# Kernel tuning notes

Measured on AMD Instinct MI355X. Metric: run time of the kernel, lower is better.

## Reference

```python
import jax, jax.numpy as jnp
import numpy as np

N = 50000
E = 400000
IN_DIM = 384
HID = 256
Q_DIM = 384
HEAD_HID = 128


def _glorot(key, shape):
    fan_in, fan_out = shape[0], shape[1]
    lim = float(np.sqrt(6.0 / (fan_in + fan_out)))
    return jax.random.uniform(key, shape, jnp.float32, -lim, lim)


def setup_inputs() -> dict:
    key = jax.random.key(0)
    ks = jax.random.split(key, 10)
    x = jax.random.normal(ks[0], (N, IN_DIM), jnp.float32)
    edge_index = jax.random.randint(ks[1], (2, E), 0, N, dtype=jnp.int64)
    q = jax.random.normal(ks[2], (Q_DIM,), jnp.float32)
    # layer 1: Linear(in_dim*2 + query_dim -> hidden)
    W1 = _glorot(ks[3], (IN_DIM * 2 + Q_DIM, HID))
    b1 = jnp.zeros((HID,), jnp.float32)
    # layer 2: Linear(hidden*2 + query_dim -> hidden)
    W2 = _glorot(ks[4], (HID * 2 + Q_DIM, HID))
    b2 = jnp.zeros((HID,), jnp.float32)
    # score head: Linear(hidden + query_dim -> 128) -> ReLU -> Linear(128 -> 1)
    Wh1 = _glorot(ks[5], (HID + Q_DIM, HEAD_HID))
    bh1 = jnp.zeros((HEAD_HID,), jnp.float32)
    Wh2 = _glorot(ks[6], (HEAD_HID, 1))
    bh2 = jnp.zeros((1,), jnp.float32)
    return {"x": x, "edge_index": edge_index, "q": q,
            "W1": W1, "b1": b1, "W2": W2, "b2": b2,
            "Wh1": Wh1, "bh1": bh1, "Wh2": Wh2, "bh2": bh2}


def _sage_layer(h, src, dst, q, W, b, n_nodes):
    # mean aggregation with self-loops: (sum_{j in N(i)} h_j + h_i) / (deg_i + 1)
    deg = jnp.zeros((n_nodes,), h.dtype).at[dst].add(1.0) + 1.0  # [N]
    agg = (jax.ops.segment_sum(h[src], dst, num_segments=n_nodes) + h) / deg[:, None]
    q_exp = jnp.broadcast_to(q, (n_nodes, q.shape[0]))
    cat = jnp.concatenate([h, agg, q_exp], axis=-1)  # [N, 2*d + q_dim]
    return jax.nn.relu(cat @ W + b)  # dropout is identity in eval mode


def reference(x, edge_index, q, W1, b1, W2, b2, Wh1, bh1, Wh2, bh2):
    src, dst = edge_index[0], edge_index[1]
    n = x.shape[0]
    h = _sage_layer(x, src, dst, q, W1, b1, n)
    h = _sage_layer(h, src, dst, q, W2, b2, n)
    q_exp = jnp.broadcast_to(q, (n, q.shape[0]))
    s = jax.nn.relu(jnp.concatenate([h, q_exp], axis=-1) @ Wh1 + bh1)
    logits = (s @ Wh2 + bh2).squeeze(-1)  # [N]
    return logits
```

## Files before the change

kernel.cpp:

```cpp
#include <hip/hip_runtime.h>
#include <cstdint>
#include <cstddef>

typedef unsigned short u16;
typedef short short8 __attribute__((ext_vector_type(8)));
typedef unsigned short u16x8 __attribute__((ext_vector_type(8)));
typedef unsigned short u16x4 __attribute__((ext_vector_type(4)));
typedef float f32x4 __attribute__((ext_vector_type(4)));

#define DEVI __device__ __forceinline__

#if defined(__has_builtin)
#if __has_builtin(__builtin_amdgcn_global_load_lds)
#define USE_GLD 1
#endif
#endif

DEVI float bf2f(u16 u) { return __uint_as_float(((unsigned)u) << 16); }
DEVI u16 f2bf(float f) {
  unsigned u = __float_as_uint(f);
  u += 0x7FFFu + ((u >> 16) & 1u);
  return (u16)(u >> 16);
}

DEVI void stage16(const u16* __restrict__ g, u16* lds_base, int lane) {
#ifdef USE_GLD
  __builtin_amdgcn_global_load_lds(
      (const __attribute__((address_space(1))) unsigned int*)g,
      (__attribute__((address_space(3))) unsigned int*)lds_base, 16, 0, 0);
#else
  *(u16x8*)(lds_base + lane * 8) = *(const u16x8*)g;
#endif
}

__global__ void build_deg(const int* __restrict__ dst, int* __restrict__ deg, int E) {
  int e = blockIdx.x * 256 + threadIdx.x;
  if (e < E) atomicAdd(&deg[dst[e]], 1);
}

__global__ __launch_bounds__(256) void scan1(const int* __restrict__ deg,
                                             int* __restrict__ pref,
                                             int* __restrict__ bsum, int Nn) {
  __shared__ int wsum[4];
  int i = blockIdx.x * 256 + threadIdx.x;
  int lane = threadIdx.x & 63, w = threadIdx.x >> 6;
  int v = (i < Nn) ? deg[i] : 0;
  int s = v;
  for (int off = 1; off < 64; off <<= 1) {
    int t = __shfl_up(s, off, 64);
    if (lane >= off) s += t;
  }
  if (lane == 63) wsum[w] = s;
  __syncthreads();
  int add = 0;
  for (int k = 0; k < w; ++k) add += wsum[k];
  int incl = s + add;
  if (i < Nn) pref[i] = incl - v;
  if (threadIdx.x == 255) bsum[blockIdx.x] = incl;
}

__global__ __launch_bounds__(256) void scan2(int* __restrict__ bsum,
                                             int* __restrict__ row_ofs,
                                             int nb, int Nn) {
  __shared__ int wsum[4];
  int t = threadIdx.x;
  int lane = t & 63, w = t >> 6;
  int v = (t < nb) ? bsum[t] : 0;
  int s = v;
  for (int off = 1; off < 64; off <<= 1) {
    int u = __shfl_up(s, off, 64);
    if (lane >= off) s += u;
  }
  if (lane == 63) wsum[w] = s;
  __syncthreads();
  int add = 0;
  for (int k = 0; k < w; ++k) add += wsum[k];
  int incl = s + add;
  if (t < nb) bsum[t] = incl - v;
  if (t == 255) row_ofs[Nn] = incl;
}

__global__ __launch_bounds__(256) void scan3(const int* __restrict__ pref,
                                             const int* __restrict__ bsum,
                                             int* __restrict__ row_ofs,
                                             int* __restrict__ cursor, int Nn) {
  int i = blockIdx.x * 256 + threadIdx.x;
  if (i < Nn) {
    int r = pref[i] + bsum[blockIdx.x];
    row_ofs[i] = r;
    cursor[i] = r;
  }
}

__global__ void csr_fill(const int* __restrict__ src, const int* __restrict__ dst,
                         int* __restrict__ cursor, int* __restrict__ col, int E) {
  int e = blockIdx.x * 256 + threadIdx.x;
  if (e < E) {
    int p = atomicAdd(&cursor[dst[e]], 1);
    col[p] = src[e];
  }
}

__global__ void pack_bt(const float* __restrict__ W, u16* __restrict__ Bt,
                        int K, int ldW, int r1) {
  int c = blockIdx.y;
  int k = blockIdx.x * 256 + threadIdx.x;
  if (k >= K) return;
  float v = (c < ldW) ? W[(size_t)k * ldW + c]
                      : W[(size_t)(r1 + k) * ldW + (c - ldW)];
  Bt[(size_t)c * K + k] = f2bf(v);
}

__global__ __launch_bounds__(384) void bias_q(
    const float* __restrict__ W, const float* __restrict__ b,
    const float* __restrict__ q, float* __restrict__ outb,
    int ld, int roff, int Kq) {
  __shared__ float part[6];
  int c = blockIdx.x;
  int t = threadIdx.x;
  float p = (t < Kq) ? q[t] * W[(size_t)(roff + t) * ld + c] : 0.0f;
  for (int off = 32; off > 0; off >>= 1) p += __shfl_down(p, off, 64);
  if ((t & 63) == 0) part[t >> 6] = p;
  __syncthreads();
  if (t == 0) {
    float acc = b[c];
    int nw = (blockDim.x + 63) >> 6;
    for (int w = 0; w < nw; ++w) acc += part[w];
    outb[c] = acc;
  }
}

#define BM 128
#define BN 128
#define BK 32


__global__ __launch_bounds__(256) void gemm_f32a(
    const float* __restrict__ A, const u16* __restrict__ Bt,
    u16* __restrict__ C, const float* __restrict__ bias,
    int M, int K, int Nc, int bias_len, int relu) {
  __shared__ __align__(16) u16 lds_a[BM * BK];
  __shared__ __align__(16) u16 lds_b[BN * BK];

  const int tid = threadIdx.x;
  const int lane = tid & 63;
  const int wave = tid >> 6;
  const int wm = wave & 1, wn = wave >> 1;
  const int row0 = blockIdx.y * BM;
  const int col0 = blockIdx.x * BN;
  const int m = lane & 15;
  const int quad = lane >> 4;
  const int csel = quad ^ ((m >> 1) & 3);

  const int rA0 = tid >> 2;
  const int rA1 = 64 + rA0;
  const int cs = tid & 3;
  const int s0 = rA0 * 4 + (cs ^ ((rA0 >> 1) & 3));
  const int s1 = rA1 * 4 + (cs ^ ((rA1 >> 1) & 3));
  int ga0 = row0 + rA0; if (ga0 >= M) ga0 = M - 1;
  int ga1 = row0 + rA1; if (ga1 >= M) ga1 = M - 1;
  const float* pa0 = A + (size_t)ga0 * K + cs * 8;
  const float* pa1 = A + (size_t)ga1 * K + cs * 8;

  const int rB0 = tid >> 2, rB1 = 64 + rB0;
  const int cB0 = (tid & 3) ^ ((rB0 >> 1) & 3);
  const int cB1 = (tid & 3) ^ ((rB1 >> 1) & 3);
  const u16* pb0 = Bt + (size_t)(col0 + rB0) * K + cB0 * 8;
  const u16* pb1 = Bt + (size_t)(col0 + rB1) * K + cB1 * 8;
  u16* ldsb_base0 = lds_b + (size_t)(wave * 64) * 8;
  u16* ldsb_base1 = lds_b + (size_t)(256 + wave * 64) * 8;

  f32x4 acc[4][4] = {};

  for (int k0 = 0; k0 < K; k0 += BK) {
    f32x4 a0a = *(const f32x4*)pa0, a0b = *(const f32x4*)(pa0 + 4); pa0 += BK;
    f32x4 a1a = *(const f32x4*)pa1, a1b = *(const f32x4*)(pa1 + 4); pa1 += BK;
    u16x8 h0, h1;
#pragma unroll
    for (int j = 0; j < 4; ++j) {
      h0[j] = f2bf(a0a[j]); h0[j + 4] = f2bf(a0b[j]);
      h1[j] = f2bf(a1a[j]); h1[j + 4] = f2bf(a1b[j]);
    }
    __syncthreads();
    stage16(pb0, ldsb_base0, lane); pb0 += BK;
    stage16(pb1, ldsb_base1, lane); pb1 += BK;
    *(u16x8*)&lds_a[s0 * 8] = h0;
    *(u16x8*)&lds_a[s1 * 8] = h1;
    __syncthreads();

    short8 af[4], bfv[4];
#pragma unroll
    for (int mt = 0; mt < 4; ++mt)
      af[mt] = *(const short8*)&lds_a[((wm * 64 + mt * 16 + m) * 4 + csel) * 8];
#pragma unroll
    for (int nt = 0; nt < 4; ++nt)
      bfv[nt] = *(const short8*)&lds_b[((wn * 64 + nt * 16 + m) * 4 + csel) * 8];
#pragma unroll
    for (int mt = 0; mt < 4; ++mt)
#pragma unroll
      for (int nt = 0; nt < 4; ++nt)
        acc[mt][nt] = __builtin_amdgcn_mfma_f32_16x16x32_bf16(
            af[mt], bfv[nt], acc[mt][nt], 0, 0, 0);
  }

#pragma unroll
  for (int nt = 0; nt < 4; ++nt) {
    int col = col0 + wn * 64 + nt * 16 + m;
    float bb = (col < bias_len) ? bias[col] : 0.0f;
#pragma unroll
    for (int mt = 0; mt < 4; ++mt)
#pragma unroll
      for (int r = 0; r < 4; ++r) {
        int row = row0 + wm * 64 + mt * 16 + quad * 4 + r;
        if (row < M) {
          float v = acc[mt][nt][r] + bb;
          if (relu) v = fmaxf(v, 0.0f);
          C[(size_t)row * Nc + col] = f2bf(v);
        }
      }
  }
}

__global__ __launch_bounds__(256) void gemm_bf16a(
    const u16* __restrict__ A, const u16* __restrict__ Bt,
    u16* __restrict__ C, const float* __restrict__ bias,
    int M, int K, int Nc, int bias_len, int relu) {
  __shared__ __align__(16) u16 lds_a[BM * BK];
  __shared__ __align__(16) u16 lds_b[BN * BK];

  const int tid = threadIdx.x;
  const int lane = tid & 63;
  const int wave = tid >> 6;
  const int wm = wave & 1, wn = wave >> 1;
  const int row0 = blockIdx.y * BM;
  const int col0 = blockIdx.x * BN;
  const int m = lane & 15;
  const int quad = lane >> 4;
  const int csel = quad ^ ((m >> 1) & 3);

  const int r0 = tid >> 2, r1 = 64 + r0;
  const int c0 = (tid & 3) ^ ((r0 >> 1) & 3);
  const int c1 = (tid & 3) ^ ((r1 >> 1) & 3);
  int ga0 = row0 + r0; if (ga0 >= M) ga0 = M - 1;
  int ga1 = row0 + r1; if (ga1 >= M) ga1 = M - 1;
  const u16* pa0 = A + (size_t)ga0 * K + c0 * 8;
  const u16* pa1 = A + (size_t)ga1 * K + c1 * 8;
  const u16* pb0 = Bt + (size_t)(col0 + r0) * K + c0 * 8;
  const u16* pb1 = Bt + (size_t)(col0 + r1) * K + c1 * 8;
  u16* la0 = lds_a + (size_t)(wave * 64) * 8;
  u16* la1 = lds_a + (size_t)(256 + wave * 64) * 8;
  u16* lb0 = lds_b + (size_t)(wave * 64) * 8;
  u16* lb1 = lds_b + (size_t)(256 + wave * 64) * 8;

  f32x4 acc[4][4] = {};

  for (int k0 = 0; k0 < K; k0 += BK) {
    __syncthreads();
    stage16(pa0, la0, lane); pa0 += BK;
    stage16(pa1, la1, lane); pa1 += BK;
    stage16(pb0, lb0, lane); pb0 += BK;
    stage16(pb1, lb1, lane); pb1 += BK;
    __syncthreads();

    short8 af[4], bfv[4];
#pragma unroll
    for (int mt = 0; mt < 4; ++mt)
      af[mt] = *(const short8*)&lds_a[((wm * 64 + mt * 16 + m) * 4 + csel) * 8];
#pragma unroll
    for (int nt = 0; nt < 4; ++nt)
      bfv[nt] = *(const short8*)&lds_b[((wn * 64 + nt * 16 + m) * 4 + csel) * 8];
#pragma unroll
    for (int mt = 0; mt < 4; ++mt)
#pragma unroll
      for (int nt = 0; nt < 4; ++nt)
        acc[mt][nt] = __builtin_amdgcn_mfma_f32_16x16x32_bf16(
            af[mt], bfv[nt], acc[mt][nt], 0, 0, 0);
  }

#pragma unroll
  for (int nt = 0; nt < 4; ++nt) {
    int col = col0 + wn * 64 + nt * 16 + m;
    float bb = (col < bias_len) ? bias[col] : 0.0f;
#pragma unroll
    for (int mt = 0; mt < 4; ++mt)
#pragma unroll
      for (int r = 0; r < 4; ++r) {
        int row = row0 + wm * 64 + mt * 16 + quad * 4 + r;
        if (row < M) {
          float v = acc[mt][nt][r] + bb;
          if (relu) v = fmaxf(v, 0.0f);
          C[(size_t)row * Nc + col] = f2bf(v);
        }
      }
  }
}

__global__ __launch_bounds__(256) void aggregate(
    const u16* __restrict__ C, const int* __restrict__ row_ofs,
    const int* __restrict__ col_idx, u16* __restrict__ H, int Nn) {
  int node = blockIdx.x * 4 + (threadIdx.x >> 6);
  if (node >= Nn) return;
  int lane = threadIdx.x & 63;
  int s = row_ofs[node], e = row_ofs[node + 1];
  float inv = 1.0f / (float)(e - s + 1);
  const u16* crow = C + (size_t)node * 512;
  u16x4 y0 = *(const u16x4*)(crow + 256 + lane * 4);
  float a0 = bf2f(y0[0]), a1 = bf2f(y0[1]), a2 = bf2f(y0[2]), a3 = bf2f(y0[3]);
  int t = s;
  for (; t + 4 <= e; t += 4) {
    int j0 = col_idx[t], j1 = col_idx[t + 1], j2 = col_idx[t + 2], j3 = col_idx[t + 3];
    u16x4 v0 = *(const u16x4*)(C + (size_t)j0 * 512 + 256 + lane * 4);
    u16x4 v1 = *(const u16x4*)(C + (size_t)j1 * 512 + 256 + lane * 4);
    u16x4 v2 = *(const u16x4*)(C + (size_t)j2 * 512 + 256 + lane * 4);
    u16x4 v3 = *(const u16x4*)(C + (size_t)j3 * 512 + 256 + lane * 4);
    a0 += bf2f(v0[0]) + bf2f(v1[0]) + bf2f(v2[0]) + bf2f(v3[0]);
    a1 += bf2f(v0[1]) + bf2f(v1[1]) + bf2f(v2[1]) + bf2f(v3[1]);
    a2 += bf2f(v0[2]) + bf2f(v1[2]) + bf2f(v2[2]) + bf2f(v3[2]);
    a3 += bf2f(v0[3]) + bf2f(v1[3]) + bf2f(v2[3]) + bf2f(v3[3]);
  }
  for (; t < e; ++t) {
    int j = col_idx[t];
    u16x4 yj = *(const u16x4*)(C + (size_t)j * 512 + 256 + lane * 4);
    a0 += bf2f(yj[0]); a1 += bf2f(yj[1]); a2 += bf2f(yj[2]); a3 += bf2f(yj[3]);
  }
  u16x4 u = *(const u16x4*)(crow + lane * 4);
  u16x4 o;
  o[0] = f2bf(fmaxf(bf2f(u[0]) + a0 * inv, 0.0f));
  o[1] = f2bf(fmaxf(bf2f(u[1]) + a1 * inv, 0.0f));
  o[2] = f2bf(fmaxf(bf2f(u[2]) + a2 * inv, 0.0f));
  o[3] = f2bf(fmaxf(bf2f(u[3]) + a3 * inv, 0.0f));
  *(u16x4*)(H + (size_t)node * 256 + lane * 4) = o;
}

__global__ __launch_bounds__(256) void head_final(
    const u16* __restrict__ S, const float* __restrict__ Wh2,
    const float* __restrict__ bh2, float* __restrict__ out, int Nn) {
  int node = blockIdx.x * 4 + (threadIdx.x >> 6);
  if (node >= Nn) return;
  int lane = threadIdx.x & 63;
  const u16* srow = S + (size_t)node * 128 + lane * 2;
  float v = bf2f(srow[0]) * Wh2[lane * 2] + bf2f(srow[1]) * Wh2[lane * 2 + 1];
  for (int off = 32; off > 0; off >>= 1) v += __shfl_down(v, off, 64);
  if (lane == 0) out[node] = v + bh2[0];
}

extern "C" void kernel_launch(void* const* d_in, const int* in_sizes, int n_in,
                              void* d_out, int out_size, void* d_ws, size_t ws_size,
                              hipStream_t stream) {
  const float* x   = (const float*)d_in[0];
  const int*   ei  = (const int*)d_in[1];
  const float* q   = (const float*)d_in[2];
  const float* W1  = (const float*)d_in[3];
  const float* b1  = (const float*)d_in[4];
  const float* W2  = (const float*)d_in[5];
  const float* b2  = (const float*)d_in[6];
  const float* Wh1 = (const float*)d_in[7];
  const float* bh1 = (const float*)d_in[8];
  const float* Wh2 = (const float*)d_in[9];
  const float* bh2 = (const float*)d_in[10];

  const int N = in_sizes[0] / 384;
  const int E = in_sizes[1] / 2;
  const int Npad = ((N + 127) / 128) * 128;
  const int* esrc = ei;
  const int* edst = ei + E;

  size_t off = 0;
  auto alloc = [&](size_t bytes) -> void* {
    void* p = (char*)d_ws + off;
    off += (bytes + 255) & ~(size_t)255;
    return p;
  };
  int* deg     = (int*)alloc((size_t)N * 4);
  int* row_ofs = (int*)alloc((size_t)(N + 1) * 4);
  int* cursor  = (int*)alloc((size_t)N * 4);
  int* colidx  = (int*)alloc((size_t)E * 4);
  int* pref    = (int*)alloc((size_t)N * 4);
  int* bsum    = (int*)alloc(256 * 4);
  u16* B1t = (u16*)alloc((size_t)512 * 384 * 2);
  u16* B2t = (u16*)alloc((size_t)512 * 256 * 2);
  u16* Bht = (u16*)alloc((size_t)128 * 256 * 2);
  float* cq1 = (float*)alloc(256 * 4);
  float* cq2 = (float*)alloc(256 * 4);
  float* cqh = (float*)alloc(128 * 4);
  u16* Cbuf = (u16*)alloc((size_t)Npad * 512 * 2);
  u16* Hbuf = (u16*)alloc((size_t)Npad * 256 * 2);

  (void)hipMemsetAsync(deg, 0, (size_t)N * 4, stream);
  int eb = (E + 255) / 256;
  int nb = (N + 255) / 256;
  build_deg<<<eb, 256, 0, stream>>>(edst, deg, E);
  scan1<<<nb, 256, 0, stream>>>(deg, pref, bsum, N);
  scan2<<<1, 256, 0, stream>>>(bsum, row_ofs, nb, N);
  scan3<<<nb, 256, 0, stream>>>(pref, bsum, row_ofs, cursor, N);
  csr_fill<<<eb, 256, 0, stream>>>(esrc, edst, cursor, colidx, E);

  pack_bt<<<dim3(2, 512), 256, 0, stream>>>(W1, B1t, 384, 256, 384);
  pack_bt<<<dim3(1, 512), 256, 0, stream>>>(W2, B2t, 256, 256, 256);
  pack_bt<<<dim3(1, 128), 256, 0, stream>>>(Wh1, Bht, 256, 128, 0);
  bias_q<<<256, 384, 0, stream>>>(W1, b1, q, cq1, 256, 768, 384);
  bias_q<<<256, 384, 0, stream>>>(W2, b2, q, cq2, 256, 512, 384);
  bias_q<<<128, 384, 0, stream>>>(Wh1, bh1, q, cqh, 128, 256, 384);

  int mb = Npad / 128;
  int nb4 = (N + 3) / 4;
  gemm_f32a<<<dim3(4, mb), 256, 0, stream>>>(x, B1t, Cbuf, cq1, N, 384, 512, 256, 0);
  aggregate<<<nb4, 256, 0, stream>>>(Cbuf, row_ofs, colidx, Hbuf, N);
  gemm_bf16a<<<dim3(4, mb), 256, 0, stream>>>(Hbuf, B2t, Cbuf, cq2, N, 256, 512, 256, 0);
  aggregate<<<nb4, 256, 0, stream>>>(Cbuf, row_ofs, colidx, Hbuf, N);
  gemm_bf16a<<<dim3(1, mb), 256, 0, stream>>>(Hbuf, Bht, Cbuf, cqh, N, 256, 128, 128, 1);
  head_final<<<nb4, 256, 0, stream>>>(Cbuf, Wh2, bh2, (float*)d_out, N);
}
```

Baseline: 419.3 us.

## Use full-width 64x512 GEMM tiles and LDS-staged coalesced epilogue stores

```diff
diff --git a/kernel.cpp b/kernel.cpp
--- a/kernel.cpp
+++ b/kernel.cpp
@@ -130,103 +130,151 @@
   }
 }
 
+#define W_NC 512
+#define ES 520
+
+#define GEMM512_COMPUTE()                                                      \
+  {                                                                            \
+    short8 bfr[8];                                                             \
+    _Pragma("unroll") for (int nt = 0; nt < 8; ++nt) bfr[nt] =                 \
+        *(const short8*)&lds_b[((wave * 128 + nt * 16 + m) * 4 + csel) * 8];   \
+    _Pragma("unroll") for (int mt = 0; mt < 4; ++mt) {                         \
+      short8 af = *(const short8*)&lds_a[((mt * 16 + m) * 4 + csel) * 8];      \
+      _Pragma("unroll") for (int nt = 0; nt < 8; ++nt)                         \
+          acc[mt][nt] = __builtin_amdgcn_mfma_f32_16x16x32_bf16(               \
+              af, bfr[nt], acc[mt][nt], 0, 0, 0);                              \
+    }                                                                          \
+  }
+
+#define GEMM512_EPILOGUE()                                                     \
+  {                                                                            \
+    u16* et = lds_b;    \
+    _Pragma("unroll") for (int mt = 0; mt < 4; ++mt) {                         \
+      __syncthreads();                                                         \
+      _Pragma("unroll") for (int nt = 0; nt < 8; ++nt) {                       \
+        int col = wave * 128 + nt * 16 + m;                                    \
+        float bb = (col < bias_len) ? bias[col] : 0.0f;                        \
+        _Pragma("unroll") for (int r = 0; r < 4; ++r) {                        \
+          float v = acc[mt][nt][r] + bb;                                       \
+          if (relu) v = fmaxf(v, 0.0f);                                        \
+          et[(quad * 4 + r) * ES + col] = f2bf(v);                             \
+        }                                                                      \
+      }                                                                        \
+      __syncthreads();                                                         \
+      _Pragma("unroll") for (int p = 0; p < 4; ++p) {                          \
+        int row_loc = p * 4 + wave;                                            \
+        int grow = row0 + mt * 16 + row_loc;                                   \
+        if (grow < M)                                                          \
+          *(u16x8*)&C[(size_t)grow * W_NC + lane * 8] =                        \
+              *(const u16x8*)&et[row_loc * ES + lane * 8];                     \
+      }                                                                        \
+    }                                                                          \
+  }
+
+#define GEMM512_B_SETUP()                                                      \
+  const u16* pbB[8];                                                           \
+  _Pragma("unroll") for (int p = 0; p < 8; ++p) {                              \
+    int L = p * 256 + tid;                                                     \
+    int c = L >> 2, qs = L & 3;                                                \
+    int g = qs ^ ((c >> 1) & 3);                                               \
+    pbB[p] = Bt + (size_t)c * K + g * 8;                                       \
+  }
+
+#define GEMM512_B_STAGE()                                                      \
+  _Pragma("unroll") for (int p = 0; p < 8; ++p) {                              \
+    stage16(pbB[p], lds_b + (size_t)(p * 256 + wave * 64) * 8, lane);          \
+    pbB[p] += 32;                                                              \
+  }
+
+__global__ __launch_bounds__(256, 2) void gemm512_f32a(
+    const float* __restrict__ A, const u16* __restrict__ Bt,
+    u16* __restrict__ C, const float* __restrict__ bias,
+    int M, int K, int bias_len, int relu) {
+  __shared__ __align__(16) u16 lds_a[64 * 32];
+  __shared__ __align__(16) u16 lds_b[512 * 32];
+
+  const int tid = threadIdx.x;
+  const int lane = tid & 63;
+  const int wave = tid >> 6;
+  const int row0 = blockIdx.x * 64;
+  const int m = lane & 15;
+  const int quad = lane >> 4;
+  const int csel = quad ^ ((m >> 1) & 3);
+
+  const int rA = tid >> 2;
+  const int qA = tid & 3;
+  const int sA = rA * 4 + (qA ^ ((rA >> 1) & 3));
+  int ga = row0 + rA; if (ga >= M) ga = M - 1;
+  const float* pa = A + (size_t)ga * K + qA * 8;
+
+  GEMM512_B_SETUP()
+
+  f32x4 acc[4][8] = {};
+
+  for (int k0 = 0; k0 < K; k0 += 32) {
+    f32x4 va = *(const f32x4*)pa, vb = *(const f32x4*)(pa + 4); pa += 32;
+    u16x8 h;
+#pragma unroll
+    for (int j = 0; j < 4; ++j) { h[j] = f2bf(va[j]); h[j + 4] = f2bf(vb[j]); }
+    __syncthreads();
+    GEMM512_B_STAGE()
+    *(u16x8*)&lds_a[sA * 8] = h;
+    __syncthreads();
+    GEMM512_COMPUTE()
+  }
+
+  GEMM512_EPILOGUE()
+}
+
+__global__ __launch_bounds__(256, 2) void gemm512_bf16a(
+    const u16* __restrict__ A, const u16* __restrict__ Bt,
+    u16* __restrict__ C, const float* __restrict__ bias,
+    int M, int K, int bias_len, int relu) {
+  __shared__ __align__(16) u16 lds_a[64 * 32];
+  __shared__ __align__(16) u16 lds_b[512 * 32];
+
+  const int tid = threadIdx.x;
+  const int lane = tid & 63;
+  const int wave = tid >> 6;
+  const int row0 = blockIdx.x * 64;
+  const int m = lane & 15;
+  const int quad = lane >> 4;
+  const int csel = quad ^ ((m >> 1) & 3);
+
+  const int rA = tid >> 2;
+  const int qA = tid & 3;
+  const int gA = qA ^ ((rA >> 1) & 3);
+  int ga = row0 + rA; if (ga >= M) ga = M - 1;
+  const u16* pa = A + (size_t)ga * K + gA * 8;
+  u16* la = lds_a + (size_t)(wave * 64) * 8;
+
+  GEMM512_B_SETUP()
+
+  f32x4 acc[4][8] = {};
+
+  for (int k0 = 0; k0 < K; k0 += 32) {
+    __syncthreads();
+    GEMM512_B_STAGE()
+    stage16(pa, la, lane); pa += 32;
+    __syncthreads();
+    GEMM512_COMPUTE()
+  }
+
+  GEMM512_EPILOGUE()
+}
+
 #define BM 128
 #define BN 128
 #define BK 32
-
-
-__global__ __launch_bounds__(256) void gemm_f32a(
-    const float* __restrict__ A, const u16* __restrict__ Bt,
-    u16* __restrict__ C, const float* __restrict__ bias,
-    int M, int K, int Nc, int bias_len, int relu) {
-  __shared__ __align__(16) u16 lds_a[BM * BK];
-  __shared__ __align__(16) u16 lds_b[BN * BK];
-
-  const int tid = threadIdx.x;
-  const int lane = tid & 63;
-  const int wave = tid >> 6;
-  const int wm = wave & 1, wn = wave >> 1;
-  const int row0 = blockIdx.y * BM;
-  const int col0 = blockIdx.x * BN;
-  const int m = lane & 15;
-  const int quad = lane >> 4;
-  const int csel = quad ^ ((m >> 1) & 3);
-
-  const int rA0 = tid >> 2;
-  const int rA1 = 64 + rA0;
-  const int cs = tid & 3;
-  const int s0 = rA0 * 4 + (cs ^ ((rA0 >> 1) & 3));
-  const int s1 = rA1 * 4 + (cs ^ ((rA1 >> 1) & 3));
-  int ga0 = row0 + rA0; if (ga0 >= M) ga0 = M - 1;
-  int ga1 = row0 + rA1; if (ga1 >= M) ga1 = M - 1;
-  const float* pa0 = A + (size_t)ga0 * K + cs * 8;
-  const float* pa1 = A + (size_t)ga1 * K + cs * 8;
-
-  const int rB0 = tid >> 2, rB1 = 64 + rB0;
-  const int cB0 = (tid & 3) ^ ((rB0 >> 1) & 3);
-  const int cB1 = (tid & 3) ^ ((rB1 >> 1) & 3);
-  const u16* pb0 = Bt + (size_t)(col0 + rB0) * K + cB0 * 8;
-  const u16* pb1 = Bt + (size_t)(col0 + rB1) * K + cB1 * 8;
-  u16* ldsb_base0 = lds_b + (size_t)(wave * 64) * 8;
-  u16* ldsb_base1 = lds_b + (size_t)(256 + wave * 64) * 8;
-
-  f32x4 acc[4][4] = {};
-
-  for (int k0 = 0; k0 < K; k0 += BK) {
-    f32x4 a0a = *(const f32x4*)pa0, a0b = *(const f32x4*)(pa0 + 4); pa0 += BK;
-    f32x4 a1a = *(const f32x4*)pa1, a1b = *(const f32x4*)(pa1 + 4); pa1 += BK;
-    u16x8 h0, h1;
-#pragma unroll
-    for (int j = 0; j < 4; ++j) {
-      h0[j] = f2bf(a0a[j]); h0[j + 4] = f2bf(a0b[j]);
-      h1[j] = f2bf(a1a[j]); h1[j + 4] = f2bf(a1b[j]);
-    }
-    __syncthreads();
-    stage16(pb0, ldsb_base0, lane); pb0 += BK;
-    stage16(pb1, ldsb_base1, lane); pb1 += BK;
-    *(u16x8*)&lds_a[s0 * 8] = h0;
-    *(u16x8*)&lds_a[s1 * 8] = h1;
-    __syncthreads();
-
-    short8 af[4], bfv[4];
-#pragma unroll
-    for (int mt = 0; mt < 4; ++mt)
-      af[mt] = *(const short8*)&lds_a[((wm * 64 + mt * 16 + m) * 4 + csel) * 8];
-#pragma unroll
-    for (int nt = 0; nt < 4; ++nt)
-      bfv[nt] = *(const short8*)&lds_b[((wn * 64 + nt * 16 + m) * 4 + csel) * 8];
-#pragma unroll
-    for (int mt = 0; mt < 4; ++mt)
-#pragma unroll
-      for (int nt = 0; nt < 4; ++nt)
-        acc[mt][nt] = __builtin_amdgcn_mfma_f32_16x16x32_bf16(
-            af[mt], bfv[nt], acc[mt][nt], 0, 0, 0);
-  }
-
-#pragma unroll
-  for (int nt = 0; nt < 4; ++nt) {
-    int col = col0 + wn * 64 + nt * 16 + m;
-    float bb = (col < bias_len) ? bias[col] : 0.0f;
-#pragma unroll
-    for (int mt = 0; mt < 4; ++mt)
-#pragma unroll
-      for (int r = 0; r < 4; ++r) {
-        int row = row0 + wm * 64 + mt * 16 + quad * 4 + r;
-        if (row < M) {
-          float v = acc[mt][nt][r] + bb;
-          if (relu) v = fmaxf(v, 0.0f);
-          C[(size_t)row * Nc + col] = f2bf(v);
-        }
-      }
-  }
-}
+#define ELD_STRIDE 136
 
 __global__ __launch_bounds__(256) void gemm_bf16a(
     const u16* __restrict__ A, const u16* __restrict__ Bt,
     u16* __restrict__ C, const float* __restrict__ bias,
     int M, int K, int Nc, int bias_len, int relu) {
-  __shared__ __align__(16) u16 lds_a[BM * BK];
-  __shared__ __align__(16) u16 lds_b[BN * BK];
+  __shared__ __align__(16) u16 lds[64 * ELD_STRIDE];
+  u16* lds_a = lds;
+  u16* lds_b = lds + BM * BK;
 
   const int tid = threadIdx.x;
   const int lane = tid & 63;
@@ -277,21 +325,37 @@
             af[mt], bfv[nt], acc[mt][nt], 0, 0, 0);
   }
 
-#pragma unroll
-  for (int nt = 0; nt < 4; ++nt) {
-    int col = col0 + wn * 64 + nt * 16 + m;
-    float bb = (col < bias_len) ? bias[col] : 0.0f;
-#pragma unroll
-    for (int mt = 0; mt < 4; ++mt)
-#pragma unroll
-      for (int r = 0; r < 4; ++r) {
-        int row = row0 + wm * 64 + mt * 16 + quad * 4 + r;
-        if (row < M) {
-          float v = acc[mt][nt][r] + bb;
-          if (relu) v = fmaxf(v, 0.0f);
-          C[(size_t)row * Nc + col] = f2bf(v);
+  {
+    const int rr = tid >> 4;
+    const int cseg = tid & 15;
+#pragma unroll
+    for (int h = 0; h < 2; ++h) {
+      __syncthreads();
+      if (wm == h) {
+#pragma unroll
+        for (int nt = 0; nt < 4; ++nt) {
+          int col_loc = wn * 64 + nt * 16 + m;
+          float bb = (col0 + col_loc < bias_len) ? bias[col0 + col_loc] : 0.0f;
+#pragma unroll
+          for (int mt = 0; mt < 4; ++mt)
+#pragma unroll
+            for (int r = 0; r < 4; ++r) {
+              float v = acc[mt][nt][r] + bb;
+              if (relu) v = fmaxf(v, 0.0f);
+              lds[(mt * 16 + quad * 4 + r) * ELD_STRIDE + col_loc] = f2bf(v);
+            }
         }
       }
+      __syncthreads();
+#pragma unroll
+      for (int p = 0; p < 4; ++p) {
+        int row_loc = p * 16 + rr;
+        int grow = row0 + h * 64 + row_loc;
+        if (grow < M)
+          *(u16x8*)&C[(size_t)grow * Nc + col0 + cseg * 8] =
+              *(const u16x8*)&lds[row_loc * ELD_STRIDE + cseg * 8];
+      }
+    }
   }
 }
 
@@ -402,11 +466,12 @@
   bias_q<<<256, 384, 0, stream>>>(W2, b2, q, cq2, 256, 512, 384);
   bias_q<<<128, 384, 0, stream>>>(Wh1, bh1, q, cqh, 128, 256, 384);
 
+  int gb64 = (N + 63) / 64;
   int mb = Npad / 128;
   int nb4 = (N + 3) / 4;
-  gemm_f32a<<<dim3(4, mb), 256, 0, stream>>>(x, B1t, Cbuf, cq1, N, 384, 512, 256, 0);
+  gemm512_f32a<<<gb64, 256, 0, stream>>>(x, B1t, Cbuf, cq1, N, 384, 256, 0);
   aggregate<<<nb4, 256, 0, stream>>>(Cbuf, row_ofs, colidx, Hbuf, N);
-  gemm_bf16a<<<dim3(4, mb), 256, 0, stream>>>(Hbuf, B2t, Cbuf, cq2, N, 256, 512, 256, 0);
+  gemm512_bf16a<<<gb64, 256, 0, stream>>>(Hbuf, B2t, Cbuf, cq2, N, 256, 256, 0);
   aggregate<<<nb4, 256, 0, stream>>>(Cbuf, row_ofs, colidx, Hbuf, N);
   gemm_bf16a<<<dim3(1, mb), 256, 0, stream>>>(Hbuf, Bht, Cbuf, cqh, N, 256, 128, 128, 1);
   head_final<<<nb4, 256, 0, stream>>>(Cbuf, Wh2, bh2, (float*)d_out, N);
```

New measurement: 377.4 us. 1.11x faster.
